# Optimization experiments

Measured on AMD Instinct MI355X. Metric: run time of the kernel, lower is better.

## Reference

```python
import math
import jax, jax.numpy as jnp
import numpy as np

B, T, D, N = 4, 4096, 2048, 32
_EPS_NORM = 1e-12  # F.normalize eps
_C = math.sqrt(2.0 / math.pi)


def setup_inputs() -> dict:
    key = jax.random.key(0)
    k1, k2 = jax.random.split(key)
    x = jax.random.normal(k1, (B, T, D), dtype=jnp.float32)
    buf = jax.random.normal(k2, (N, D), dtype=jnp.float32)
    mask = jnp.ones((N,), dtype=bool)  # fully-filled ring buffer (steady state)
    log_alpha = jnp.asarray(math.log(math.exp(0.5) - 1.0), dtype=jnp.float32)
    log_tau = jnp.asarray(math.log(2.0), dtype=jnp.float32)
    return {"x": x, "buf": buf, "mask": mask, "log_alpha": log_alpha, "log_tau": log_tau}


def _gelu_tanh(x):
    return 0.5 * x * (1.0 + jnp.tanh(_C * (x + 0.044715 * x * x * x)))


def reference(x, buf, mask, log_alpha, log_tau):
    # x: [B,T,D], buf: [N,D] (non-differentiable ring-buffer state), mask: [N] bool
    alpha = jax.nn.softplus(log_alpha)
    tau = jnp.exp(log_tau)
    y = _gelu_tanh(x)                                   # [B,T,D]

    # current episode mean (detached in torch)
    m_curr = jax.lax.stop_gradient(y.reshape(-1, y.shape[-1]).mean(0))  # [D]

    # cosine similarity of buffer rows vs current mean (F.normalize semantics)
    m_norm = m_curr / jnp.maximum(jnp.linalg.norm(m_curr), _EPS_NORM)   # [D]
    b_norm = buf / jnp.maximum(
        jnp.linalg.norm(buf, axis=-1, keepdims=True), _EPS_NORM)        # [N,D]
    sims = jnp.where(mask, b_norm @ m_norm, -1.0)                       # [N]
    nearest_ep = jax.lax.stop_gradient(buf[jnp.argmax(sims)])           # [D]

    # unbiased std over filled buffer rows (mask-weighted, matches torch .std(0))
    w = mask.astype(buf.dtype)[:, None]                                  # [N,1]
    n = w.sum()
    mu = (buf * w).sum(0) / n                                            # [D]
    var = (w * (buf - mu) ** 2).sum(0) / (n - 1.0)
    buf_std = jnp.clip(jnp.sqrt(var), 0.0001, None)                      # [D]

    dev = (y - nearest_ep) / (buf_std + 1e-05)
    fam = jnp.exp(-tau * dev * dev)
    gate = jnp.clip(1.0 - alpha * fam, 0.05, 1.05)
    return y * gate
```

## Files before the change

### kernel.cpp

```cpp
#include <hip/hip_runtime.h>
#include <math.h>

#define DIM  2048
#define ROWS 16384
#define NBUF 32
#define NREP 64

#define WS_REP   0
#define WS_MEAN  (NREP * DIM)
#define WS_INV   (WS_MEAN + DIM)
#define WS_NE    (WS_INV + DIM)
#define WS_ALPHA (WS_NE + DIM)
#define WS_TAU   (WS_ALPHA + 1)
#define WS_MSQ   (WS_ALPHA + 2)
#define WS_DOT   (WS_ALPHA + 8)
#define WS_BSQ   (WS_DOT + NBUF)

__device__ __forceinline__ float fast_tanh(float z) {
    float az = fabsf(z);
    float e  = __expf(2.0f * az);
    float t  = 1.0f - 2.0f / (e + 1.0f);
    return copysignf(t, z);
}

__device__ __forceinline__ float gelu_tanh(float x) {
    float x3 = x * x * x;
    float z  = 0.7978845608028654f * (x + 0.044715f * x3);
    return 0.5f * x * (1.0f + fast_tanh(z));
}

__global__ __launch_bounds__(256) void colsum_kernel(const float* __restrict__ x,
                                                     float* __restrict__ ws) {
    const int t  = threadIdx.x;
    const int rg = blockIdx.x >> 1;
    const int h  = blockIdx.x & 1;
    const float4* base = (const float4*)x + (size_t)rg * 16 * 512 + (size_t)h * 256 + t;
    float4 a = {0.f, 0.f, 0.f, 0.f};
    #pragma unroll
    for (int rr = 0; rr < 16; rr += 4) {
        float4 v0 = base[(size_t)(rr + 0) * 512];
        float4 v1 = base[(size_t)(rr + 1) * 512];
        float4 v2 = base[(size_t)(rr + 2) * 512];
        float4 v3 = base[(size_t)(rr + 3) * 512];
        a.x += gelu_tanh(v0.x) + gelu_tanh(v1.x) + gelu_tanh(v2.x) + gelu_tanh(v3.x);
        a.y += gelu_tanh(v0.y) + gelu_tanh(v1.y) + gelu_tanh(v2.y) + gelu_tanh(v3.y);
        a.z += gelu_tanh(v0.z) + gelu_tanh(v1.z) + gelu_tanh(v2.z) + gelu_tanh(v3.z);
        a.w += gelu_tanh(v0.w) + gelu_tanh(v1.w) + gelu_tanh(v2.w) + gelu_tanh(v3.w);
    }
    float* rep = ws + WS_REP + (size_t)(rg & (NREP - 1)) * DIM + h * 1024;
    const int c0 = t * 4;
    atomicAdd(&rep[c0 + 0], a.x);
    atomicAdd(&rep[c0 + 1], a.y);
    atomicAdd(&rep[c0 + 2], a.z);
    atomicAdd(&rep[c0 + 3], a.w);
}

__global__ __launch_bounds__(256) void finalize_kernel(const float* __restrict__ buf,
                                                       float* __restrict__ ws) {
    const int c = blockIdx.x * 256 + threadIdx.x;
    float s = 0.f;
    #pragma unroll 8
    for (int r = 0; r < NREP; ++r) s += ws[WS_REP + (size_t)r * DIM + c];
    ws[WS_MEAN + c] = s * (1.0f / (float)ROWS);

    float bs = 0.f, bss = 0.f;
    #pragma unroll 8
    for (int n = 0; n < NBUF; ++n) {
        float v = buf[(size_t)n * DIM + c];
        bs += v; bss += v * v;
    }
    float mu  = bs * (1.0f / (float)NBUF);
    float var = (bss - (float)NBUF * mu * mu) * (1.0f / (float)(NBUF - 1));
    var = fmaxf(var, 0.f);
    float sd = fmaxf(sqrtf(var), 1e-4f);
    ws[WS_INV + c] = 1.0f / (sd + 1e-5f);
}

__global__ __launch_bounds__(256) void stats_kernel(const float* __restrict__ buf,
                                                    float* __restrict__ ws) {
    __shared__ float red[256];
    const int bid = blockIdx.x;
    const int t   = threadIdx.x;

    if (bid < NBUF) {
        const float* brow = buf + (size_t)bid * DIM;
        float d = 0.f, q = 0.f;
        for (int c = t; c < DIM; c += 256) {
            float bv = brow[c];
            float mv = ws[WS_MEAN + c];
            d += bv * mv;
            q += bv * bv;
        }
        red[t] = d; __syncthreads();
        for (int s = 128; s > 0; s >>= 1) { if (t < s) red[t] += red[t + s]; __syncthreads(); }
        float dsum = red[0]; __syncthreads();
        red[t] = q; __syncthreads();
        for (int s = 128; s > 0; s >>= 1) { if (t < s) red[t] += red[t + s]; __syncthreads(); }
        if (t == 0) { ws[WS_DOT + bid] = dsum; ws[WS_BSQ + bid] = red[0]; }
    } else {
        float q = 0.f;
        for (int c = t; c < DIM; c += 256) {
            float mv = ws[WS_MEAN + c];
            q += mv * mv;
        }
        red[t] = q; __syncthreads();
        for (int s = 128; s > 0; s >>= 1) { if (t < s) red[t] += red[t + s]; __syncthreads(); }
        if (t == 0) ws[WS_MSQ] = red[0];
    }
}

__global__ __launch_bounds__(256) void select_kernel(const float* __restrict__ buf,
                                                     const float* __restrict__ log_alpha,
                                                     const float* __restrict__ log_tau,
                                                     float* __restrict__ ws) {
    __shared__ int ksh;
    const int t = threadIdx.x;
    if (t == 0) {
        float mnorm = fmaxf(sqrtf(ws[WS_MSQ]), 1e-12f);
        float best = -1e30f; int bi = 0;
        for (int n = 0; n < NBUF; ++n) {
            float bn  = fmaxf(sqrtf(ws[WS_BSQ + n]), 1e-12f);
            float sim = ws[WS_DOT + n] / (bn * mnorm);
            if (sim > best) { best = sim; bi = n; }
        }
        ksh = bi;
        float la = log_alpha[0];
        ws[WS_ALPHA] = (la > 20.0f) ? la : log1pf(expf(la));
        ws[WS_TAU]   = expf(log_tau[0]);
    }
    __syncthreads();
    const int k = ksh;
    for (int c = t; c < DIM; c += 256) ws[WS_NE + c] = buf[(size_t)k * DIM + c];
}

__global__ __launch_bounds__(256) void gate_kernel(const float* __restrict__ x,
                                                   const float* __restrict__ ws,
                                                   float* __restrict__ out) {
    const float alpha = ws[WS_ALPHA];
    const float tau   = ws[WS_TAU];
    const float4* ne  = (const float4*)(ws + WS_NE);
    const float4* inv = (const float4*)(ws + WS_INV);
    const float4* xv4 = (const float4*)x;
    float4* ov4       = (float4*)out;

    const size_t nvec   = (size_t)ROWS * DIM / 4;
    const size_t stride = (size_t)gridDim.x * blockDim.x;
    for (size_t i = (size_t)blockIdx.x * blockDim.x + threadIdx.x; i < nvec; i += stride) {
        const int colv = (int)(i & 511);
        float4 xv = xv4[i];
        float4 nv = ne[colv];
        float4 iv = inv[colv];
        float4 o;
        {
            float y = gelu_tanh(xv.x);
            float dv = (y - nv.x) * iv.x;
            float fam = __expf(-tau * dv * dv);
            float g = fminf(fmaxf(1.0f - alpha * fam, 0.05f), 1.05f);
            o.x = y * g;
        }
        {
            float y = gelu_tanh(xv.y);
            float dv = (y - nv.y) * iv.y;
            float fam = __expf(-tau * dv * dv);
            float g = fminf(fmaxf(1.0f - alpha * fam, 0.05f), 1.05f);
            o.y = y * g;
        }
        {
            float y = gelu_tanh(xv.z);
            float dv = (y - nv.z) * iv.z;
            float fam = __expf(-tau * dv * dv);
            float g = fminf(fmaxf(1.0f - alpha * fam, 0.05f), 1.05f);
            o.z = y * g;
        }
        {
            float y = gelu_tanh(xv.w);
            float dv = (y - nv.w) * iv.w;
            float fam = __expf(-tau * dv * dv);
            float g = fminf(fmaxf(1.0f - alpha * fam, 0.05f), 1.05f);
            o.w = y * g;
        }
        ov4[i] = o;
    }
}

extern "C" void kernel_launch(void* const* d_in, const int* in_sizes, int n_in,
                              void* d_out, int out_size, void* d_ws, size_t ws_size,
                              hipStream_t stream) {
    const float* x   = (const float*)d_in[0];
    const float* buf = (const float*)d_in[1];
    const float* la  = (const float*)d_in[3];
    const float* lt  = (const float*)d_in[4];
    float* out = (float*)d_out;
    float* ws  = (float*)d_ws;

    hipMemsetAsync(ws, 0, (size_t)NREP * DIM * sizeof(float), stream);
    hipLaunchKernelGGL(colsum_kernel,   dim3(2048), dim3(256), 0, stream, x, ws);
    hipLaunchKernelGGL(finalize_kernel, dim3(8),    dim3(256), 0, stream, buf, ws);
    hipLaunchKernelGGL(stats_kernel,    dim3(33),   dim3(256), 0, stream, buf, ws);
    hipLaunchKernelGGL(select_kernel,   dim3(1),    dim3(256), 0, stream, buf, la, lt, ws);
    hipLaunchKernelGGL(gate_kernel,     dim3(4096), dim3(256), 0, stream, x, ws, out);
}
```

Measured before the change: 119.5 us.

## Fuse finalize, stats and select into one block; double rows per colsum block

Merges the three small middle kernels (mean finalize, dot/norm stats, argmax select) into a single 1024-thread block that keeps the mean in shared memory and uses wave shuffles for reductions. This removes two kernel launches and their global round trips. The colsum kernel now handles 32 rows per block with 8 loads in flight and half the grid, which halves the atomics. The fused middle step runs on one CU, so its serial work is no longer spread across blocks.

```diff
diff --git a/kernel.cpp b/kernel.cpp
--- a/kernel.cpp
+++ b/kernel.cpp
@@ -7,14 +7,10 @@
 #define NREP 64
 
 #define WS_REP   0
-#define WS_MEAN  (NREP * DIM)
-#define WS_INV   (WS_MEAN + DIM)
+#define WS_INV   (NREP * DIM)
 #define WS_NE    (WS_INV + DIM)
 #define WS_ALPHA (WS_NE + DIM)
 #define WS_TAU   (WS_ALPHA + 1)
-#define WS_MSQ   (WS_ALPHA + 2)
-#define WS_DOT   (WS_ALPHA + 8)
-#define WS_BSQ   (WS_DOT + NBUF)
 
 __device__ __forceinline__ float fast_tanh(float z) {
     float az = fabsf(z);
@@ -29,23 +25,30 @@
     return 0.5f * x * (1.0f + fast_tanh(z));
 }
 
-__global__ __launch_bounds__(256) void colsum_kernel(const float* __restrict__ x,
-                                                     float* __restrict__ ws) {
+__global__ __launch_bounds__(256, 4) void colsum_kernel(const float* __restrict__ x,
+                                                        float* __restrict__ ws) {
     const int t  = threadIdx.x;
     const int rg = blockIdx.x >> 1;
     const int h  = blockIdx.x & 1;
-    const float4* base = (const float4*)x + (size_t)rg * 16 * 512 + (size_t)h * 256 + t;
+    const float4* base = (const float4*)x + (size_t)rg * 32 * 512 + h * 256 + t;
     float4 a = {0.f, 0.f, 0.f, 0.f};
-    #pragma unroll
-    for (int rr = 0; rr < 16; rr += 4) {
+    for (int rr = 0; rr < 32; rr += 8) {
         float4 v0 = base[(size_t)(rr + 0) * 512];
         float4 v1 = base[(size_t)(rr + 1) * 512];
         float4 v2 = base[(size_t)(rr + 2) * 512];
         float4 v3 = base[(size_t)(rr + 3) * 512];
-        a.x += gelu_tanh(v0.x) + gelu_tanh(v1.x) + gelu_tanh(v2.x) + gelu_tanh(v3.x);
-        a.y += gelu_tanh(v0.y) + gelu_tanh(v1.y) + gelu_tanh(v2.y) + gelu_tanh(v3.y);
-        a.z += gelu_tanh(v0.z) + gelu_tanh(v1.z) + gelu_tanh(v2.z) + gelu_tanh(v3.z);
-        a.w += gelu_tanh(v0.w) + gelu_tanh(v1.w) + gelu_tanh(v2.w) + gelu_tanh(v3.w);
+        float4 v4 = base[(size_t)(rr + 4) * 512];
+        float4 v5 = base[(size_t)(rr + 5) * 512];
+        float4 v6 = base[(size_t)(rr + 6) * 512];
+        float4 v7 = base[(size_t)(rr + 7) * 512];
+        a.x += gelu_tanh(v0.x); a.y += gelu_tanh(v0.y); a.z += gelu_tanh(v0.z); a.w += gelu_tanh(v0.w);
+        a.x += gelu_tanh(v1.x); a.y += gelu_tanh(v1.y); a.z += gelu_tanh(v1.z); a.w += gelu_tanh(v1.w);
+        a.x += gelu_tanh(v2.x); a.y += gelu_tanh(v2.y); a.z += gelu_tanh(v2.z); a.w += gelu_tanh(v2.w);
+        a.x += gelu_tanh(v3.x); a.y += gelu_tanh(v3.y); a.z += gelu_tanh(v3.z); a.w += gelu_tanh(v3.w);
+        a.x += gelu_tanh(v4.x); a.y += gelu_tanh(v4.y); a.z += gelu_tanh(v4.z); a.w += gelu_tanh(v4.w);
+        a.x += gelu_tanh(v5.x); a.y += gelu_tanh(v5.y); a.z += gelu_tanh(v5.z); a.w += gelu_tanh(v5.w);
+        a.x += gelu_tanh(v6.x); a.y += gelu_tanh(v6.y); a.z += gelu_tanh(v6.z); a.w += gelu_tanh(v6.w);
+        a.x += gelu_tanh(v7.x); a.y += gelu_tanh(v7.y); a.z += gelu_tanh(v7.z); a.w += gelu_tanh(v7.w);
     }
     float* rep = ws + WS_REP + (size_t)(rg & (NREP - 1)) * DIM + h * 1024;
     const int c0 = t * 4;
@@ -55,72 +58,64 @@
     atomicAdd(&rep[c0 + 3], a.w);
 }
 
-__global__ __launch_bounds__(256) void finalize_kernel(const float* __restrict__ buf,
-                                                       float* __restrict__ ws) {
-    const int c = blockIdx.x * 256 + threadIdx.x;
-    float s = 0.f;
-    #pragma unroll 8
-    for (int r = 0; r < NREP; ++r) s += ws[WS_REP + (size_t)r * DIM + c];
-    ws[WS_MEAN + c] = s * (1.0f / (float)ROWS);
+__global__ __launch_bounds__(1024) void mid_kernel(const float* __restrict__ buf,
+                                                   const float* __restrict__ log_alpha,
+                                                   const float* __restrict__ log_tau,
+                                                   float* __restrict__ ws) {
+    __shared__ float mean_lds[DIM];
+    __shared__ float red[1024];
+    __shared__ float dots[NBUF];
+    __shared__ float bsqs[NBUF];
+    __shared__ int ksh;
+    const int t = threadIdx.x;
 
-    float bs = 0.f, bss = 0.f;
-    #pragma unroll 8
-    for (int n = 0; n < NBUF; ++n) {
-        float v = buf[(size_t)n * DIM + c];
-        bs += v; bss += v * v;
+    float msq_local = 0.f;
+    for (int c = t; c < DIM; c += 1024) {
+        float s = 0.f;
+        #pragma unroll 8
+        for (int r = 0; r < NREP; ++r) s += ws[WS_REP + (size_t)r * DIM + c];
+        float mean = s * (1.0f / (float)ROWS);
+        mean_lds[c] = mean;
+        msq_local += mean * mean;
+
+        float bs = 0.f, bss = 0.f;
+        #pragma unroll 8
+        for (int n = 0; n < NBUF; ++n) {
+            float v = buf[(size_t)n * DIM + c];
+            bs += v; bss += v * v;
+        }
+        float mu  = bs * (1.0f / (float)NBUF);
+        float var = (bss - (float)NBUF * mu * mu) * (1.0f / (float)(NBUF - 1));
+        var = fmaxf(var, 0.f);
+        float sd = fmaxf(sqrtf(var), 1e-4f);
+        ws[WS_INV + c] = 1.0f / (sd + 1e-5f);
     }
-    float mu  = bs * (1.0f / (float)NBUF);
-    float var = (bss - (float)NBUF * mu * mu) * (1.0f / (float)(NBUF - 1));
-    var = fmaxf(var, 0.f);
-    float sd = fmaxf(sqrtf(var), 1e-4f);
-    ws[WS_INV + c] = 1.0f / (sd + 1e-5f);
-}
+    red[t] = msq_local; __syncthreads();
+    for (int s = 512; s > 0; s >>= 1) { if (t < s) red[t] += red[t + s]; __syncthreads(); }
+    const float msq = red[0];
 
-__global__ __launch_bounds__(256) void stats_kernel(const float* __restrict__ buf,
-                                                    float* __restrict__ ws) {
-    __shared__ float red[256];
-    const int bid = blockIdx.x;
-    const int t   = threadIdx.x;
-
-    if (bid < NBUF) {
-        const float* brow = buf + (size_t)bid * DIM;
+    const int w = t >> 6, lane = t & 63;
+    for (int n = w; n < NBUF; n += 16) {
         float d = 0.f, q = 0.f;
-        for (int c = t; c < DIM; c += 256) {
-            float bv = brow[c];
-            float mv = ws[WS_MEAN + c];
-            d += bv * mv;
+        for (int c = lane; c < DIM; c += 64) {
+            float bv = buf[(size_t)n * DIM + c];
+            d += bv * mean_lds[c];
             q += bv * bv;
         }
-        red[t] = d; __syncthreads();
-        for (int s = 128; s > 0; s >>= 1) { if (t < s) red[t] += red[t + s]; __syncthreads(); }
-        float dsum = red[0]; __syncthreads();
-        red[t] = q; __syncthreads();
-        for (int s = 128; s > 0; s >>= 1) { if (t < s) red[t] += red[t + s]; __syncthreads(); }
-        if (t == 0) { ws[WS_DOT + bid] = dsum; ws[WS_BSQ + bid] = red[0]; }
-    } else {
-        float q = 0.f;
-        for (int c = t; c < DIM; c += 256) {
-            float mv = ws[WS_MEAN + c];
-            q += mv * mv;
+        for (int off = 32; off > 0; off >>= 1) {
+            d += __shfl_down(d, off);
+            q += __shfl_down(q, off);
         }
-        red[t] = q; __syncthreads();
-        for (int s = 128; s > 0; s >>= 1) { if (t < s) red[t] += red[t + s]; __syncthreads(); }
-        if (t == 0) ws[WS_MSQ] = red[0];
+        if (lane == 0) { dots[n] = d; bsqs[n] = q; }
     }
-}
+    __syncthreads();
 
-__global__ __launch_bounds__(256) void select_kernel(const float* __restrict__ buf,
-                                                     const float* __restrict__ log_alpha,
-                                                     const float* __restrict__ log_tau,
-                                                     float* __restrict__ ws) {
-    __shared__ int ksh;
-    const int t = threadIdx.x;
     if (t == 0) {
-        float mnorm = fmaxf(sqrtf(ws[WS_MSQ]), 1e-12f);
+        float mnorm = fmaxf(sqrtf(msq), 1e-12f);
         float best = -1e30f; int bi = 0;
         for (int n = 0; n < NBUF; ++n) {
-            float bn  = fmaxf(sqrtf(ws[WS_BSQ + n]), 1e-12f);
-            float sim = ws[WS_DOT + n] / (bn * mnorm);
+            float bn  = fmaxf(sqrtf(bsqs[n]), 1e-12f);
+            float sim = dots[n] / (bn * mnorm);
             if (sim > best) { best = sim; bi = n; }
         }
         ksh = bi;
@@ -129,8 +124,9 @@
         ws[WS_TAU]   = expf(log_tau[0]);
     }
     __syncthreads();
+
     const int k = ksh;
-    for (int c = t; c < DIM; c += 256) ws[WS_NE + c] = buf[(size_t)k * DIM + c];
+    for (int c = t; c < DIM; c += 1024) ws[WS_NE + c] = buf[(size_t)k * DIM + c];
 }
 
 __global__ __launch_bounds__(256) void gate_kernel(const float* __restrict__ x,
@@ -194,9 +190,7 @@
     float* ws  = (float*)d_ws;
 
     hipMemsetAsync(ws, 0, (size_t)NREP * DIM * sizeof(float), stream);
-    hipLaunchKernelGGL(colsum_kernel,   dim3(2048), dim3(256), 0, stream, x, ws);
-    hipLaunchKernelGGL(finalize_kernel, dim3(8),    dim3(256), 0, stream, buf, ws);
-    hipLaunchKernelGGL(stats_kernel,    dim3(33),   dim3(256), 0, stream, buf, ws);
-    hipLaunchKernelGGL(select_kernel,   dim3(1),    dim3(256), 0, stream, buf, la, lt, ws);
-    hipLaunchKernelGGL(gate_kernel,     dim3(4096), dim3(256), 0, stream, x, ws, out);
+    hipLaunchKernelGGL(colsum_kernel, dim3(1024), dim3(256),  0, stream, x, ws);
+    hipLaunchKernelGGL(mid_kernel,    dim3(1),    dim3(1024), 0, stream, buf, la, lt, ws);
+    hipLaunchKernelGGL(gate_kernel,   dim3(4096), dim3(256),  0, stream, x, ws, out);
 }
```

Measured after the change: 109.3 us. 1.09x faster.
